# Kernel tuning notes

Measured on AMD Instinct MI355X. Metric: run time of the kernel, lower is better.

Reference implementation:

```python
import jax, jax.numpy as jnp
import numpy as np
from math import factorial

N_NODES = 20000
N_EDGES = 80000
NUM_GRAPHS = 64
NUM_NEIGHBORS = 3.8
POOL_NODES = 4.0  # num_nodes=4 constant in source forward

# ---------------- real Wigner 3j (e3nn-style, Frobenius norm 1) ----------------

def _w3j_complex(j1, j2, j3, m1, m2, m3):
    if m1 + m2 + m3 != 0:
        return 0.0
    t1 = j2 - m1 - j3; t2 = j1 + m2 - j3; t3 = j1 + j2 - j3
    t4 = j1 - m1; t5 = j2 + m2
    tmin = max(0, t1, t2); tmax = min(t3, t4, t5)
    if tmin > tmax:
        return 0.0
    s = 0.0
    for t in range(tmin, tmax + 1):
        s += (-1.0) ** t / (factorial(t) * factorial(t - t1) * factorial(t - t2)
                            * factorial(t3 - t) * factorial(t4 - t) * factorial(t5 - t))
    tri = (factorial(j1 + j2 - j3) * factorial(j1 - j2 + j3) * factorial(-j1 + j2 + j3)
           / factorial(j1 + j2 + j3 + 1))
    norm = np.sqrt(tri * factorial(j1 + m1) * factorial(j1 - m1) * factorial(j2 + m2)
                   * factorial(j2 - m2) * factorial(j3 + m3) * factorial(j3 - m3))
    return (-1.0) ** (j1 - j2 - m3) * norm * s


def _real_basis(l):
    U = np.zeros((2 * l + 1, 2 * l + 1), dtype=np.complex128)
    U[l, l] = 1.0
    for m in range(1, l + 1):
        U[l + m, l + m] = (-1) ** m / np.sqrt(2.0)
        U[l + m, l - m] = 1.0 / np.sqrt(2.0)
        U[l - m, l - m] = 1j / np.sqrt(2.0)
        U[l - m, l + m] = -1j * (-1) ** m / np.sqrt(2.0)
    return U

_W3J_CACHE = {}

def w3j(l1, l2, l3):
    key = (l1, l2, l3)
    if key not in _W3J_CACHE:
        C = np.zeros((2 * l1 + 1, 2 * l2 + 1, 2 * l3 + 1), dtype=np.complex128)
        for m1 in range(-l1, l1 + 1):
            for m2 in range(-l2, l2 + 1):
                m3 = -(m1 + m2)
                if -l3 <= m3 <= l3:
                    C[m1 + l1, m2 + l2, m3 + l3] = _w3j_complex(l1, l2, l3, m1, m2, m3)
        C = np.einsum('ia,jb,kc,abc->ijk', _real_basis(l1), _real_basis(l2), _real_basis(l3), C)
        C = np.real((-1j) ** (l1 + l2 + l3) * C)
        _W3J_CACHE[key] = jnp.asarray(C, dtype=jnp.float32)
    return _W3J_CACHE[key]

# ---------------- irreps bookkeeping ----------------
SH        = [(1, 0, 1), (1, 1, -1), (1, 2, 1), (1, 3, -1)]            # 1x0e+1x1o+1x2e+1x3o (dim 16)
GATE1_IN  = [(16,0,1),(16,0,-1),(8,0,1),(8,0,-1),(8,0,1),(8,0,-1),(16,1,-1),(16,1,1)]  # dim 160
GATE1_OUT = [(16,0,1),(16,0,1),(16,1,-1),(16,1,1)]                     # dim 128
GATE2_IN  = [(16,0,1),(16,0,-1),(6,0,1),(6,0,-1),(6,0,1),(6,0,-1),(12,1,-1),(12,1,1)]  # dim 128
GATE2_OUT = [(16,0,1),(16,0,1),(12,1,-1),(12,1,1)]                     # dim 104
OUT_FINAL = [(1, 0, 1)]


def slices(irreps):
    out = []; o = 0
    for m, l, p in irreps:
        d = m * (2 * l + 1); out.append((o, o + d)); o += d
    return out


def tp_paths(ir1, ir2, iro):
    paths = []
    for i1, (m1, l1, p1) in enumerate(ir1):
        for i2, (m2, l2, p2) in enumerate(ir2):
            for io, (mo, lo, po) in enumerate(iro):
                if po == p1 * p2 and abs(l1 - l2) <= lo <= l1 + l2:
                    paths.append((i1, i2, io))
    fan = [0] * len(iro)
    for i1, i2, io in paths:
        fan[io] += ir1[i1][0] * ir2[i2][0]
    numel = sum(ir1[i1][0] * ir2[i2][0] * iro[io][0] for i1, i2, io in paths)
    return paths, fan, numel


def tensor_product(x1, x2, weights, ir1, ir2, iro):
    # FullyConnectedTensorProduct, component norm, element path normalization
    paths, fan, numel = tp_paths(ir1, ir2, iro)
    s1, s2 = slices(ir1), slices(ir2)
    E = x1.shape[0]
    out_parts = [jnp.zeros((E, m * (2 * l + 1)), x1.dtype) for m, l, p in iro]
    wofs = 0
    for i1, i2, io in paths:
        m1, l1, _ = ir1[i1]; m2, l2, _ = ir2[i2]; mo, lo, _ = iro[io]
        n = m1 * m2 * mo
        w = weights[:, wofs:wofs + n].reshape(E, m1, m2, mo); wofs += n
        a = x1[:, s1[i1][0]:s1[i1][1]].reshape(E, m1, 2 * l1 + 1)
        b = x2[:, s2[i2][0]:s2[i2][1]].reshape(E, m2, 2 * l2 + 1)
        C = w3j(l1, l2, lo)
        pw = np.sqrt((2 * lo + 1) / fan[io])
        seg = jnp.einsum('eui,evj,ijk,euvw->ewk', a, b, C, w) * pw
        out_parts[io] = out_parts[io] + seg.reshape(E, mo * (2 * lo + 1))
    return jnp.concatenate(out_parts, axis=1)

# ---------------- activations / gate ----------------
_xs = np.linspace(-8.0, 8.0, 100001)
_pdf = np.exp(-0.5 * _xs ** 2) / np.sqrt(2 * np.pi)
TANH_NORM = float(1.0 / np.sqrt(np.sum(np.tanh(_xs) ** 2 * _pdf) * (_xs[1] - _xs[0])))
SQRT2 = float(np.sqrt(2.0))
ACT = {'relu': lambda t: jnp.maximum(t, 0.0) * SQRT2,
       'abs':  lambda t: jnp.abs(t),
       'tanh': lambda t: jnp.tanh(t) * TANH_NORM}


def gate_fn(x, scalars, gates, gated):
    o = 0; outs = []
    for m, a in scalars:
        outs.append(ACT[a](x[:, o:o + m])); o += m
    gv = []
    for m, a in gates:
        gv.append(ACT[a](x[:, o:o + m])); o += m
    g = jnp.concatenate(gv, axis=-1)
    gi = 0
    for m, l in gated:
        d = 2 * l + 1
        feat = x[:, o:o + m * d].reshape(-1, m, d)
        outs.append((feat * g[:, gi:gi + m, None]).reshape(-1, m * d))
        o += m * d; gi += m
    return jnp.concatenate(outs, axis=-1)

# ---------------- edge features ----------------

def sh_component(v):
    # real spherical harmonics l=0..3, 'component' normalization, unit input
    x, y, z = v[:, 0], v[:, 1], v[:, 2]
    s3, s5, s15 = np.sqrt(3.0), np.sqrt(5.0), np.sqrt(15.0)
    s7, s42, s70, s105 = np.sqrt(7.0), np.sqrt(42.0), np.sqrt(70.0), np.sqrt(105.0)
    Y0 = jnp.ones_like(x)[:, None]
    Y1 = jnp.stack([s3 * y, s3 * z, s3 * x], -1)
    Y2 = jnp.stack([s15 * x * y, s15 * y * z, 0.5 * s5 * (3 * z * z - 1.0),
                    s15 * x * z, 0.5 * s15 * (x * x - y * y)], -1)
    Y3 = jnp.stack([0.25 * s70 * y * (3 * x * x - y * y), s105 * x * y * z,
                    0.25 * s42 * y * (5 * z * z - 1.0), 0.5 * s7 * z * (5 * z * z - 3.0),
                    0.25 * s42 * x * (5 * z * z - 1.0), 0.5 * s105 * z * (x * x - y * y),
                    0.25 * s70 * x * (x * x - 3 * y * y)], -1)
    return jnp.concatenate([Y0, Y1, Y2, Y3], -1)  # [E,16]


def soft_one_hot(r):
    # soft_one_hot_linspace(start=0.5,end=2.5,number=3,basis='smooth_finite',cutoff=True)
    values = np.linspace(0.5, 2.5, 5)[1:-1]
    step = values[1] - values[0]
    diff = (r[:, None] - values) / step
    def f(u):
        return jnp.where(u > 0, jnp.exp(-1.0 / jnp.where(u > 0, u, 1.0)), 0.0)
    y = 1.14136 * np.exp(2.0) * f(diff + 1.0) * f(1.0 - diff)
    return y * np.sqrt(3.0)


def fc(x, w1, w2):
    # e3nn FullyConnectedNet([3,256,numel], relu)
    h = jnp.maximum(x @ (w1 / np.sqrt(w1.shape[0])), 0.0) * SQRT2
    return h @ (w2 / np.sqrt(w2.shape[0]))


def convolution(node_feats, edge_src, edge_dst, edge_attr, edge_scalars, w1, w2, ir_in, ir_out, n_nodes):
    weight = fc(edge_scalars, w1, w2)                                   # [E, numel]
    ef = tensor_product(node_feats[edge_src], edge_attr, weight, ir_in, SH, ir_out)
    return jax.ops.segment_sum(ef, edge_dst, num_segments=n_nodes) / np.sqrt(NUM_NEIGHBORS)


def _forward(pos, w1_1, w2_1, w1_2, w2_2, w1_3, w2_3, edge_src, edge_dst, batch):
    N = pos.shape[0]
    vec = pos[edge_src] - pos[edge_dst]
    r = jnp.sqrt(jnp.sum(vec * vec, axis=1) + 1e-12)
    unit = vec / r[:, None]
    edge_attr = sh_component(unit)
    edge_scalars = soft_one_hot(r)
    x = jax.ops.segment_sum(edge_attr, edge_dst, num_segments=N) / np.sqrt(NUM_NEIGHBORS)
    x = convolution(x, edge_src, edge_dst, edge_attr, edge_scalars, w1_1, w2_1, SH, GATE1_IN, N)
    x = gate_fn(x, [(16, 'relu'), (16, 'abs')], [(8, 'relu'), (8, 'tanh'), (8, 'relu'), (8, 'tanh')], [(16, 1), (16, 1)])
    x = convolution(x, edge_src, edge_dst, edge_attr, edge_scalars, w1_2, w2_2, GATE1_OUT, GATE2_IN, N)
    x = gate_fn(x, [(16, 'relu'), (16, 'abs')], [(6, 'relu'), (6, 'tanh'), (6, 'relu'), (6, 'tanh')], [(12, 1), (12, 1)])
    x = convolution(x, edge_src, edge_dst, edge_attr, edge_scalars, w1_3, w2_3, GATE2_OUT, OUT_FINAL, N)
    x = jax.ops.segment_sum(x, batch, num_segments=NUM_GRAPHS) / np.sqrt(POOL_NODES)
    return jax.nn.sigmoid(x)


def setup_inputs():
    key = jax.random.key(0)
    ks = jax.random.split(key, 10)
    pos = jax.random.normal(ks[0], (N_NODES, 3), jnp.float32) * 1.5
    edge_src = jax.random.randint(ks[1], (N_EDGES,), 0, N_NODES)
    edge_dst = jax.random.randint(ks[2], (N_EDGES,), 0, N_NODES)
    batch = jnp.sort(jax.random.randint(ks[3], (N_NODES,), 0, NUM_GRAPHS))
    _, _, n1 = tp_paths(SH, SH, GATE1_IN)
    _, _, n2 = tp_paths(GATE1_OUT, SH, GATE2_IN)
    _, _, n3 = tp_paths(GATE2_OUT, SH, OUT_FINAL)
    w1_1 = jax.random.normal(ks[4], (3, 256), jnp.float32)
    w2_1 = jax.random.normal(ks[5], (256, n1), jnp.float32)
    w1_2 = jax.random.normal(ks[6], (3, 256), jnp.float32)
    w2_2 = jax.random.normal(ks[7], (256, n2), jnp.float32)
    w1_3 = jax.random.normal(ks[8], (3, 256), jnp.float32)
    w2_3 = jax.random.normal(ks[9], (256, n3), jnp.float32)
    return {'pos': pos, 'w1_1': w1_1, 'w2_1': w2_1, 'w1_2': w1_2, 'w2_2': w2_2,
            'w1_3': w1_3, 'w2_3': w2_3, 'edge_src': edge_src, 'edge_dst': edge_dst, 'batch': batch}


def reference(pos, w1_1, w2_1, w1_2, w2_2, w1_3, w2_3, edge_src, edge_dst, batch):
    return _forward(pos, w1_1, w2_1, w1_2, w2_2, w1_3, w2_3, edge_src, edge_dst, batch)
```

## Files before the change

### kernel.cpp

```cpp
#include <hip/hip_runtime.h>
#include <math.h>

#define NNODE 20000
#define NEDGE 80000
#define NGRAPH 64

#define OFF_TANH  656
#define OFF_CNT   660
#define OFF_GSUM  664
#define OFF_HIST  7680
#define OFF_OFFS  9728
#define OFF_CUR   11784
#define OFF_EATTR 14336
#define OFF_RBUF  1294336
#define OFF_EINFO 1374336
#define OFF_X0    1694336
#define OFF_Y1    2014336
#define OFF_Y2    5214336
#define OFF_X1    7774336
#define OFF_X2    10334336
#define OFF_TAB   12414336

#define T000 0
#define T110 1
// ... 277 lines not shown
__constant__ ColMetaT< 1,  3,  44> CMETA3 = gen_colmeta_< 1,  3,  44>(OSEG3, HPATHS3, HCORES3);

struct CItem { short aoff, boff, n1, n2, cofs, jstep, woff, pad; };
struct CArr1 { CItem it[31]; };
constexpr CArr1 gen_c1_(){
  CArr1 a{}; int s=0;
  for(int cn=0;cn<13;cn++){
    CoreD cd=HCORES1[cn];
    int n1=2*cd.l1+1,n2=2*cd.l2+1,n3=2*cd.l3+1;
    for(int k=0;k<n3;k++){
      a.it[s]=CItem{cd.a_off,cd.b_off,(short)n1,(short)n2,(short)(cd.tab+k),(short)n3,(short)(cd.coff+k),0};
      s++;
    }
  }
  return a;
}
__constant__ CArr1 CIT1 = gen_c1_();

struct Fam { short b_off, tab, n1, n2, n3, goff; };
constexpr Fam GF2[6]={
  {0,T000,1,1,1,0},{1,T011,1,3,3,1},{0,T101,3,1,3,4},
  {1,T110,3,3,1,13},{1,T111,3,3,3,16},{4,T121,3,5,3,25}};
constexpr Fam GF3[2]={{0,T000,1,1,1,0},{1,T110,3,3,1,1}};
struct CoreG { short fam,a_off,m1,coff; };
constexpr CoreG CG2[12]={
  {0,0,16,0},{1,0,16,16},{0,16,16,64},{1,16,16,80},
  {2,32,16,128},{3,32,16,176},{4,32,16,192},{5,32,16,240},
  {2,80,16,288},{3,80,16,336},{4,80,16,352},{5,80,16,400}};
constexpr CoreG CG3[3]={{0,0,16,0},{0,16,16,16},{1,32,12,32}};

struct GItem { short boff, cofs, n2, jstep; };
template<int NG> struct GArrT { GItem it[NG]; };
template<int NG,int NF>
constexpr GArrT<NG> gen_g_(const Fam (&F)[NF]){
  GArrT<NG> a{}; int s=0;
  for(int f=0;f<NF;f++){
    for(int i=0;i<F[f].n1;i++)for(int k=0;k<F[f].n3;k++){
      a.it[s]=GItem{F[f].b_off,(short)(F[f].tab + i*F[f].n2*F[f].n3 + k),F[f].n2,F[f].n3};
      s++;
    }
  }
  return a;
}
__constant__ GArrT<34> GIT2=gen_g_<34>(GF2);
__constant__ GArrT<4>  GIT3=gen_g_<4>(GF3);

struct OItem { short aoff, gofs, n1, n3, woff, pad; };
template<int NO> struct OArrT { OItem it[NO]; };
template<int NO,int NC,int NF>
constexpr OArrT<NO> gen_o_(const CoreG (&C)[NC], const Fam (&F)[NF]){
  OArrT<NO> a{}; int s=0;
  for(int cn=0;cn<NC;cn++){
    Fam f=F[C[cn].fam];
    for(int k=0;k<f.n3;k++)for(int u=0;u<C[cn].m1;u++){
      a.it[s]=OItem{(short)(C[cn].a_off+u*f.n1),(short)(f.goff+k),f.n1,f.n3,
                    (short)(C[cn].coff+k*C[cn].m1+u),0};
      s++;
    }
  }
  return a;
}
__constant__ OArrT<448> OIT2=gen_o_<448,12,6>(CG2,GF2);
__constant__ OArrT<44>  OIT3=gen_o_<44,3,2>(CG3,GF3);

template<int CNT,int N3,int NCOLS>
__device__ __forceinline__ void apply1_col(const Ent2* __restrict__ ep, const float* __restrict__ T0,
    const float* __restrict__ crb, float fr, float&a0,float&a1,float&a2){
  const float* tja=T0+ep[0].jb;
  float wv[CNT];
  #pragma unroll
  for(int t=0;t<CNT;t++){
    float w0=tja[t], w1=tja[t+NCOLS];
    wv[t]=w0+fr*(w1-w0);
  }
  #pragma unroll
  for(int t=0;t<CNT;t++){
    const float* cr=crb+ep[t].cb;
    a0=fmaf(wv[t],cr[0],a0);
    if constexpr(N3==3){ a1=fmaf(wv[t],cr[1],a1); a2=fmaf(wv[t],cr[2],a2); }
  }
}
__device__ __forceinline__ void apply1_dyn(const Ent2* __restrict__ ep, int cnt, int n3,
    const float* __restrict__ T0, const float* __restrict__ crb, float fr, int NCOLS,
    float&a0,float&a1,float&a2){
  const float* tja=T0+ep[0].jb;
  for(int t=0;t<cnt;t++){
    float w0=tja[t], w1=tja[t+NCOLS];
    float w=w0+fr*(w1-w0);
    const float* cr=crb+ep[t].cb;
    a0=fmaf(w,cr[0],a0);
    if(n3==3){ a1=fmaf(w,cr[1],a1); a2=fmaf(w,cr[2],a2); }
  }
}
template<int CNT,int N3,int NCOLS>
__device__ __forceinline__ void apply2_col(const Ent2* __restrict__ ep, const float* __restrict__ T0,
    const float* __restrict__ crb, float fr, float&a0,float&a1,float&a2){
  #pragma unroll
  for(int t=0;t<CNT;t++){
    const float* cr=crb+ep[t].cb;
    const float* tj=T0+ep[t].jb;
    #pragma unroll
    for(int uu=0;uu<16;uu+=4){
      float4 w0=*(const float4*)(tj+uu);
      float4 w1=*(const float4*)(tj+NCOLS+uu);
      float w;
      if constexpr(N3==1){
        float4 cv=*(const float4*)(cr+uu);
        w=w0.x+fr*(w1.x-w0.x); a0=fmaf(w,cv.x,a0);
        w=w0.y+fr*(w1.y-w0.y); a0=fmaf(w,cv.y,a0);
        w=w0.z+fr*(w1.z-w0.z); a0=fmaf(w,cv.z,a0);
        w=w0.w+fr*(w1.w-w0.w); a0=fmaf(w,cv.w,a0);
      } else {
        float4 c0=*(const float4*)(cr+uu);
        float4 c1=*(const float4*)(cr+16+uu);
        float4 c2=*(const float4*)(cr+32+uu);
        w=w0.x+fr*(w1.x-w0.x); a0=fmaf(w,c0.x,a0); a1=fmaf(w,c1.x,a1); a2=fmaf(w,c2.x,a2);
        w=w0.y+fr*(w1.y-w0.y); a0=fmaf(w,c0.y,a0); a1=fmaf(w,c1.y,a1); a2=fmaf(w,c2.y,a2);
        w=w0.z+fr*(w1.z-w0.z); a0=fmaf(w,c0.z,a0); a1=fmaf(w,c1.z,a1); a2=fmaf(w,c2.z,a2);
        w=w0.w+fr*(w1.w-w0.w); a0=fmaf(w,c0.w,a0); a1=fmaf(w,c1.w,a1); a2=fmaf(w,c2.w,a2);
      }
    }
  }
}
__device__ __forceinline__ void apply2_dyn(const Ent2* __restrict__ ep, int cnt, int n3,
    const float* __restrict__ T0, const float* __restrict__ crb, float fr, int NCOLS,
    float&a0,float&a1,float&a2){
  for(int t=0;t<cnt;t++){
    const float* cr=crb+ep[t].cb;
    const float* tj=T0+ep[t].jb;
    #pragma unroll
    for(int uu=0;uu<16;uu+=4){
      float4 w0=*(const float4*)(tj+uu);
      float4 w1=*(const float4*)(tj+NCOLS+uu);
      float w;
      if(n3==1){
        float4 cv=*(const float4*)(cr+uu);
        w=w0.x+fr*(w1.x-w0.x); a0=fmaf(w,cv.x,a0);
        w=w0.y+fr*(w1.y-w0.y); a0=fmaf(w,cv.y,a0);
        w=w0.z+fr*(w1.z-w0.z); a0=fmaf(w,cv.z,a0);
        w=w0.w+fr*(w1.w-w0.w); a0=fmaf(w,cv.w,a0);
      } else {
        float4 c0=*(const float4*)(cr+uu);
        float4 c1=*(const float4*)(cr+16+uu);
        float4 c2=*(const float4*)(cr+32+uu);
        w=w0.x+fr*(w1.x-w0.x); a0=fmaf(w,c0.x,a0); a1=fmaf(w,c1.x,a1); a2=fmaf(w,c2.x,a2);
        w=w0.y+fr*(w1.y-w0.y); a0=fmaf(w,c0.y,a0); a1=fmaf(w,c1.y,a1); a2=fmaf(w,c2.y,a2);
        w=w0.z+fr*(w1.z-w0.z); a0=fmaf(w,c0.z,a0); a1=fmaf(w,c1.z,a1); a2=fmaf(w,c2.z,a2);
        w=w0.w+fr*(w1.w-w0.w); a0=fmaf(w,c0.w,a0); a1=fmaf(w,c1.w,a1); a2=fmaf(w,c2.w,a2);
      }
    }
  }
}

template<int JT>
__device__ __forceinline__ void ldw_(float* w, const float* p){
  if constexpr(JT==2) *(float2*)w = *(const float2*)p;
  else if constexpr(JT==4) *(float4*)w = *(const float4*)p;
  else { *(float4*)w=*(const float4*)p; *(float4*)(w+4)=*(const float4*)(p+4); }
}
template<int JT>
__device__ __forceinline__ void table_gemm(const float* __restrict__ W2, float* __restrict__ tab,
    int NCOLS, float scale, const float* __restrict__ PW, const int* __restrict__ NJ,
    int jb, const float (*__restrict__ sh_h)[8], int r0, int R){
  float acc[8][JT];
  #pragma unroll
  for(int k=0;k<8;k++)
    #pragma unroll
    for(int u=0;u<JT;u++) acc[k][u]=0.0f;
  const float* w2p=W2+jb;
  float w0[JT], w1[JT];
  ldw_<JT>(w0, w2p);
  ldw_<JT>(w1, w2p+NCOLS);
  for(int c=0;c<256;c+=2){
    int cp0=(c+2<256)?(c+2):255;
    int cp1=(c+3<256)?(c+3):255;
    float n0[JT], n1[JT];
    ldw_<JT>(n0, w2p+(size_t)cp0*NCOLS);
    ldw_<JT>(n1, w2p+(size_t)cp1*NCOLS);
    float h0[8], h1[8];
    *(float4*)&h0[0]=*(const float4*)&sh_h[c][0];
    *(float4*)&h0[4]=*(const float4*)&sh_h[c][4];
    *(float4*)&h1[0]=*(const float4*)&sh_h[c+1][0];
    *(float4*)&h1[4]=*(const float4*)&sh_h[c+1][4];
    #pragma unroll
    for(int k=0;k<8;k++)
      #pragma unroll
      for(int u=0;u<JT;u++)
        acc[k][u]=fmaf(h0[k],w0[u],acc[k][u]);
    #pragma unroll
    for(int k=0;k<8;k++)
      #pragma unroll
      for(int u=0;u<JT;u++)
        acc[k][u]=fmaf(h1[k],w1[u],acc[k][u]);
    #pragma unroll
    for(int u=0;u<JT;u++){ w0[u]=n0[u]; w1[u]=n1[u]; }
  }
  #pragma unroll
  for(int u=0;u<JT;u++){
    float cs=scale*PW[jb+u];
    int jn=NJ[jb+u];
    #pragma unroll
    for(int k=0;k<8;k++){
      int ri=r0+k;
      if(ri<R) tab[(size_t)ri*NCOLS+jn]=acc[k][u]*cs;
    }
  }
}

__global__ __launch_bounds__(256) void k_front(
    const float* __restrict__ W1_1, const float* __restrict__ W2_1, float* __restrict__ T1,
    const float* __restrict__ W1_2, const float* __restrict__ W2_2, float* __restrict__ T2,
    const float* __restrict__ W1_3, const float* __restrict__ W2_3, float* __restrict__ T3,
    const float* __restrict__ pos, const int* __restrict__ esrc, const int* __restrict__ edst,
    int R, int NR, int NXT, float* __restrict__ ws){
  __shared__ float sh_h[256][8];
  int bid=blockIdx.x;
  int tid=threadIdx.x;
  int NT2=7*NXT;

  if(bid<NT2+2*NXT){
    int jb0, jlim, xt;
    const float* W1; const float* W2; float* tab; int NCOLS; float scale;
    const float* PW; const int* NJ;
    if(bid<NT2){
      int s=bid/NXT; xt=bid-s*NXT; jb0=s*512; jlim=(jb0+512<3328)?(jb0+512):3328;
      W1=W1_2; W2=W2_2; tab=T2; NCOLS=3328; scale=INV_SQRT_NEIGH; PW=PWC2.v; NJ=CMETA2.newj;
    } else if(bid<NT2+NXT){
      xt=bid-NT2; jb0=0; jlim=272;
      W1=W1_1; W2=W2_1; tab=T1; NCOLS=272; scale=INV_SQRT_NEIGH; PW=PWC1.v; NJ=CMETA1.newj;
    } else {
      xt=bid-NT2-NXT; jb0=0; jlim=44;
      W1=W1_3; W2=W2_3; tab=T3; NCOLS=44; scale=INV_SQRT_NEIGH*0.5f; PW=PWC3.v; NJ=CMETA3.newj;
    }
    int r0=xt*8;
    {
      int c=tid;
      float wa=W1[c], wb=W1[256+c], wc=W1[512+c];
      const float A=(float)(1.14136*7.38905609893065*1.7320508075688772);
      #pragma unroll
      for(int k=0;k<8;k++){
        int ri=r0+k;
        float r=0.5f+2.0f*(float)ri/(float)NR;
        float sv[3];
        #pragma unroll
        for(int j=0;j<3;j++){
          float v=1.0f+0.5f*(float)j;
          float diff=(r-v)*2.0f;
          float u1=diff+1.0f, u2=1.0f-diff;
          float f1=(u1>0.0f)? expf(-1.0f/u1):0.0f;
          float f2=(u2>0.0f)? expf(-1.0f/u2):0.0f;
          sv[j]=A*f1*f2;
        }
        float hv=sv[0]*wa+sv[1]*wb+sv[2]*wc;
        hv=fmaxf(hv*0.5773502691896258f,0.0f)*(SQRT2F*0.0625f);
        sh_h[c][k]=hv;
      }
    }
    __syncthreads();
    int jb=jb0+tid*2;
    if(jb+2<=jlim)
      table_gemm<2>(W2,tab,NCOLS,scale,PW,NJ,jb,sh_h,r0,R);
    return;
  }
  bid-=NT2+2*NXT;

  if(bid==0){
    __shared__ double red[256];
    double loc=0.0;
    for(int i=tid;i<=100000;i+=256){
      float x=-8.0f+16.0f*(float)i/100000.0f;
      float th=tanhf(x);
      float pdf=expf(-0.5f*x*x)*0.3989422804014327f;
      loc += (double)(th*th*pdf);
    }
    red[tid]=loc; __syncthreads();
    for(int s=128;s>0;s>>=1){ if(tid<s) red[tid]+=red[tid+s]; __syncthreads(); }
    if(tid==0) ws[OFF_TANH]=(float)(1.0/sqrt(red[0]*(16.0/100000.0)));
    return;
  }
  bid-=1;

  if(bid<313){
    int e=bid*256+tid;
    if(e>=NEDGE) return;
    float* eattr=ws+OFF_EATTR;
    float* x0=ws+OFF_X0;
    int s=esrc[e], d=edst[e];
    float x=pos[3*s]-pos[3*d], y=pos[3*s+1]-pos[3*d+1], z=pos[3*s+2]-pos[3*d+2];
    float r=sqrtf(x*x+y*y+z*z+1e-12f);
    float iv=1.0f/r; x*=iv; y*=iv; z*=iv;
    const float s3=1.7320508075688772f, s5=2.2360679774997896f, s15=3.872983346207417f;
    const float s7=2.6457513110645907f, s42=6.48074069840786f, s70=8.366600265340756f, s105=10.246950765959598f;
    float Y[16];
    Y[0]=1.0f;
    Y[1]=s3*y; Y[2]=s3*z; Y[3]=s3*x;
    Y[4]=s15*x*y; Y[5]=s15*y*z; Y[6]=0.5f*s5*(3.0f*z*z-1.0f); Y[7]=s15*x*z; Y[8]=0.5f*s15*(x*x-y*y);
    Y[9]=0.25f*s70*y*(3.0f*x*x-y*y); Y[10]=s105*x*y*z; Y[11]=0.25f*s42*y*(5.0f*z*z-1.0f);
    Y[12]=0.5f*s7*z*(5.0f*z*z-3.0f); Y[13]=0.25f*s42*x*(5.0f*z*z-1.0f);
    Y[14]=0.5f*s105*z*(x*x-y*y); Y[15]=0.25f*s70*x*(x*x-3.0f*y*y);
    float4* ep=(float4*)(eattr+(size_t)e*16);
    ep[0]=make_float4(Y[0],Y[1],Y[2],Y[3]);
    ep[1]=make_float4(Y[4],Y[5],Y[6],Y[7]);
    ep[2]=make_float4(Y[8],Y[9],Y[10],Y[11]);
    ep[3]=make_float4(Y[12],Y[13],Y[14],Y[15]);
    #pragma unroll
    for(int i=0;i<16;i++)
      atomicAdd(&x0[(size_t)d*16+i], Y[i]*INV_SQRT_NEIGH);
    ws[OFF_RBUF+e]=r;
    if(r>0.5f && r<2.5f){
      float t=(r-0.5f)*((float)NR*0.5f);
      int i0=min((int)t, NR-1);
      atomicAdd((int*)(ws+OFF_HIST)+i0, 1);
    }
    return;
  }
  bid-=313;

  {
    float4* dst=(float4*)(ws+OFF_Y1);
    size_t n4=(size_t)(OFF_X1-OFF_Y1)/4;
    float4 z4=make_float4(0.f,0.f,0.f,0.f);
    for(size_t i=(size_t)bid*256+tid; i<n4; i+=(size_t)256*256)
      dst[i]=z4;
  }
}

__global__ void k_scan(float* __restrict__ ws, int NR){
  __shared__ int sd[2048];
  int t=threadIdx.x;
  int* hist=(int*)(ws+OFF_HIST);
  int* offs=(int*)(ws+OFF_OFFS);
  int i1=t, i2=t+1024;
  sd[i1]=(i1<NR)? hist[i1]:0;
  sd[i2]=(i2<NR)? hist[i2]:0;
  __syncthreads();
  for(int d=1; d<2048; d<<=1){
    int v1=(i1>=d)? sd[i1-d]:0;
    int v2=(i2>=d)? sd[i2-d]:0;
    __syncthreads();
    sd[i1]+=v1; sd[i2]+=v2;
    __syncthreads();
  }
  if(i1<NR) offs[i1]=(i1==0)?0:sd[i1-1];
  if(i2<NR) offs[i2]=sd[i2-1];
  if(t==0){ offs[NR]=sd[NR-1]; *((int*)(ws+OFF_CNT))=sd[NR-1]; }
}

__global__ void k_scatter(const int* __restrict__ esrc, const int* __restrict__ edst,
                          float* __restrict__ ws, int NR){
  int e=blockIdx.x*256+threadIdx.x;
  if(e>=NEDGE) return;
  float r=ws[OFF_RBUF+e];
  if(!(r>0.5f && r<2.5f)) return;
  float t=(r-0.5f)*((float)NR*0.5f);
  int i0=min((int)t, NR-1);
  int* offs=(int*)(ws+OFF_OFFS);
  int* cur=(int*)(ws+OFF_CUR);
  int p=offs[i0]+atomicAdd(&cur[i0],1);
  int4 v; v.x=esrc[e]; v.y=edst[e]; v.z=e; v.w=__float_as_int(t);
  ((int4*)(ws+OFF_EINFO))[p]=v;
}

template<int CONV,int DY,int D_IN,int D_OUT,int CSTRIDE,int NCOL,int NCOLS,bool FINAL>
__global__ __launch_bounds__(256,4) void k_conv(
    const float* __restrict__ xin, const float* __restrict__ TAB,
    float* __restrict__ yout, const int* __restrict__ batchp,
    float* __restrict__ ws, int NR)
{
  constexpr int APAD = D_IN+4;
  constexpr int NGP  = (CONV==2)?36:4;
  constexpr int YST  = (CONV==3)?132:4;
  constexpr int NGV  = (CONV==2)?32:((CONV==3)?24:1);
  __shared__ float sh_a[8][APAD];
  __shared__ float sh_b[8][20];
  __shared__ float sh_core[8][CSTRIDE];
  __shared__ float sh_g[8][NGP];
  __shared__ float sh_gv[8][NGV];
  __shared__ float sh_y[8][YST];
  __shared__ float sh_red[8];
  __shared__ int sh_src[8], sh_dst[8], sh_eid[8];
  __shared__ float sh_t[8];

  int tid=threadIdx.x;
  int nact=*(const int*)(ws+OFF_CNT);
  int base=blockIdx.x*8;
  if(base>=nact) return;
  int ne=min(8, nact-base);

  if(tid<8){
    int src=0,dst=0,eid=-1; float tv=0.0f;
    if(tid<ne){
      int4 v=((const int4*)(ws+OFF_EINFO))[base+tid];
      src=v.x; dst=v.y; eid=v.z; tv=__int_as_float(v.w);
    }
    sh_src[tid]=src; sh_dst[tid]=dst; sh_eid[tid]=eid; sh_t[tid]=tv;
    if constexpr(CONV==3) sh_red[tid]=0.0f;
  }
  __syncthreads();

  if(tid<32){
    int idx=tid>>2, c4=tid&3;
    int eid=sh_eid[idx];
    float4 v=make_float4(0.f,0.f,0.f,0.f);
    if(eid>=0) v=((const float4*)(ws+OFF_EATTR+(size_t)eid*16))[c4];
    *(float4*)&sh_b[idx][c4*4]=v;
  }
  if constexpr(CONV==1){
    if(tid>=32 && tid<64){
      int t2=tid-32; int idx=t2>>2, c4=t2&3;
      float4 v=make_float4(0.f,0.f,0.f,0.f);
      if(sh_eid[idx]>=0) v=((const float4*)(xin+(size_t)sh_src[idx]*16))[c4];
      *(float4*)&sh_a[idx][c4*4]=v;
    }
  } else {
    constexpr int YQ=DY/4;
    for(int z=tid; z<8*YQ; z+=256){
      int idx=z/YQ, c4=z-idx*YQ;
      float4 v=make_float4(0.f,0.f,0.f,0.f);
      if(sh_eid[idx]>=0) v=((const float4*)(xin+(size_t)sh_src[idx]*DY))[c4];
      if constexpr(CONV==2) *(float4*)&sh_core[idx][c4*4]=v;
      else                  *(float4*)&sh_y[idx][c4*4]=v;
    }
  }
  __syncthreads();

  if constexpr(CONV==1){
    constexpr int NIT=31;
    for(int z=tid; z<8*NIT; z+=256){
      int idx=z/NIT, rem=z-idx*NIT;
      CItem it=CIT1.it[rem];
      float acc=0.0f;
      for(int i=0;i<it.n1;i++){
        float av=sh_a[idx][it.aoff+i];
        int cb=it.cofs + i*it.n2*it.jstep;
        for(int j=0;j<it.n2;j++)
          acc += av*sh_b[idx][it.boff+j]*W3JC.v[cb + j*it.jstep];
      }
      sh_core[idx][it.woff]=acc;
    }
    __syncthreads();
  } else {
    float TN=ws[OFF_TANH];
    for(int z=tid; z<8*NGV; z+=256){
      int idx=z/NGV, m=z-idx*NGV;
      const float* yr=(CONV==2)? &sh_core[idx][0] : &sh_y[idx][0];
      float u=yr[32+m];
      bool th=(CONV==2)? (((m>>3)&1)!=0) : (((m/6)&1)!=0);
      sh_gv[idx][m]= th? tanhf(u)*TN : fmaxf(u,0.0f)*SQRT2F;
    }
    constexpr int NG=(CONV==2)?34:4;
    for(int z=tid; z<8*NG; z+=256){
      int idx=z/NG, rem=z-idx*NG;
      GItem it=(CONV==2)? GIT2.it[rem] : GIT3.it[rem];
      float acc=0.0f;
      for(int j=0;j<it.n2;j++)
        acc += sh_b[idx][it.boff+j]*W3JC.v[it.cofs + j*it.jstep];
      sh_g[idx][rem]=acc;
    }
    __syncthreads();
    for(int z=tid; z<8*D_IN; z+=256){
      int idx=z/D_IN, o=z-idx*D_IN;
      const float* yr=(CONV==2)? &sh_core[idx][0] : &sh_y[idx][0];
      float val;
      if(o<16) val=fmaxf(yr[o],0.0f)*SQRT2F;
      else if(o<32) val=fabsf(yr[o]);
      else {
        if constexpr(CONV==2){
          int gi=(o<80)? (o-32)/3 : 16+(o-80)/3;
          val=yr[o+32]*sh_gv[idx][gi];
        } else {
          int gi=(o<68)? (o-32)/3 : 12+(o-68)/3;
          val=yr[o+24]*sh_gv[idx][gi];
        }
      }
      sh_a[idx][o]=val;
    }
    __syncthreads();
    constexpr int NO=(CONV==2)?448:44;
    for(int z=tid; z<8*NO; z+=256){
      int idx=z/NO, rem=z-idx*NO;
      OItem it=(CONV==2)? OIT2.it[rem] : OIT3.it[rem];
      float acc=0.0f;
      #pragma unroll 3
      for(int i=0;i<it.n1;i++)
        acc += sh_a[idx][it.aoff+i]*sh_g[idx][it.gofs + i*it.n3];
      sh_core[idx][it.woff]=acc;
    }
    __syncthreads();
  }

  if constexpr(CONV==3){
    if(tid<88){
      int e3=tid&7, c=tid>>3;
      float tv=sh_t[e3];
      int i0=min((int)tv, NR-1);
      float fr=tv-(float)i0;
      const float* tj=TAB+(size_t)i0*NCOLS + c*4;
      float4 w0=*(const float4*)tj;
      float4 w1=*(const float4*)(tj+NCOLS);
      float4 cv=*(const float4*)(&sh_core[e3][c*4]);
      float p;
      p  = (w0.x+fr*(w1.x-w0.x))*cv.x;
      p += (w0.y+fr*(w1.y-w0.y))*cv.y;
      p += (w0.z+fr*(w1.z-w0.z))*cv.z;
      p += (w0.w+fr*(w1.w-w0.w))*cv.w;
      atomicAdd(&sh_red[e3], p);
    }
    __syncthreads();
    if(tid<ne) atomicAdd(&ws[OFF_GSUM+batchp[sh_dst[tid]]], sh_red[tid]);
  } else {
    int e=tid&7;
    float tv=sh_t[e];
    int i0=min((int)tv, NR-1);
    float fr=tv-(float)i0;
    const float* T0=TAB+(size_t)i0*NCOLS;
    const float* crb=&sh_core[e][0];
    int dstv=sh_dst[e];
    bool act=(e<ne);

    for(int q=tid; q<8*NCOL; q+=256){
      int c=q>>3;
      int s0,s1,ob,n3;
      const Ent2* entp;
      if constexpr(CONV==1){ s0=CMETA1.cidx[c]; s1=CMETA1.cidx[c+1]; ob=CMETA1.obase[c]; n3=CMETA1.n3c[c]; entp=CMETA1.ent; }
      else                 { s0=CMETA2.cidx[c]; s1=CMETA2.cidx[c+1]; ob=CMETA2.obase[c]; n3=CMETA2.n3c[c]; entp=CMETA2.ent; }
      int cnt=s1-s0;
      if(!cnt) continue;
      float a0=0.0f,a1=0.0f,a2=0.0f;
      const Ent2* ep=entp+s0;
      if constexpr(CONV==1){
        if(n3==1){
          switch(cnt){
            case 4: apply1_col<4,1,272>(ep,T0,crb,fr,a0,a1,a2); break;
            default: apply1_dyn(ep,cnt,1,T0,crb,fr,272,a0,a1,a2); break;
          }
        } else {
          switch(cnt){
            case 6: apply1_col<6,3,272>(ep,T0,crb,fr,a0,a1,a2); break;
            case 3: apply1_col<3,3,272>(ep,T0,crb,fr,a0,a1,a2); break;
            default: apply1_dyn(ep,cnt,3,T0,crb,fr,272,a0,a1,a2); break;
          }
        }
      } else {
        if(n3==1){
          switch(cnt){
            case 3: apply2_col<3,1,3328>(ep,T0,crb,fr,a0,a1,a2); break;
            case 1: apply2_col<1,1,3328>(ep,T0,crb,fr,a0,a1,a2); break;
            default: apply2_dyn(ep,cnt,1,T0,crb,fr,3328,a0,a1,a2); break;
          }
        } else {
          switch(cnt){
            case 5: apply2_col<5,3,3328>(ep,T0,crb,fr,a0,a1,a2); break;
            case 3: apply2_col<3,3,3328>(ep,T0,crb,fr,a0,a1,a2); break;
            default: apply2_dyn(ep,cnt,3,T0,crb,fr,3328,a0,a1,a2); break;
          }
        }
      }
      if(act){
        float* yp=&yout[(size_t)dstv*D_OUT+ob];
        atomicAdd(yp, a0);
        if(n3==3){ atomicAdd(yp+1, a1); atomicAdd(yp+2, a2); }
      }
    }
  }
}

__global__ void k_sig(const float* __restrict__ ws, float* __restrict__ out){
  int g=threadIdx.x;
  if(g<NGRAPH){
    float v=ws[OFF_GSUM+g];
    out[g]=1.0f/(1.0f+expf(-v));
  }
}

extern "C" void kernel_launch(void* const* d_in, const int* in_sizes, int n_in,
                              void* d_out, int out_size, void* d_ws, size_t ws_size,
                              hipStream_t stream){
  const float* pos =(const float*)d_in[0];
  const float* w1_1=(const float*)d_in[1];
  const float* w2_1=(const float*)d_in[2];
  const float* w1_2=(const float*)d_in[3];
  const float* w2_2=(const float*)d_in[4];
  const float* w1_3=(const float*)d_in[5];
  const float* w2_3=(const float*)d_in[6];
  const int* esrc=(const int*)d_in[7];
  const int* edst=(const int*)d_in[8];
  const int* batch=(const int*)d_in[9];
  float* ws=(float*)d_ws;
  float* out=(float*)d_out;

  long availRows = ((long)(ws_size/4) - (long)OFF_TAB)/3644L;
  int R = (availRows < 1025L)? (int)availRows : 1025;
  if(R < 9) R = 9;
  int NR = R-1;
  int NXT = (R+7)/8;
  float* TAB1 = ws + OFF_TAB;
  float* TAB2 = TAB1 + (size_t)R*272;
  float* TAB3 = TAB2 + (size_t)R*3328;

  hipMemsetAsync(ws+OFF_CNT, 0, (size_t)(728-OFF_CNT)*sizeof(float), stream);
  hipMemsetAsync(ws+OFF_HIST, 0, (size_t)(13832-OFF_HIST)*sizeof(float), stream);
  hipMemsetAsync(ws+OFF_X0, 0, (size_t)(OFF_Y1-OFF_X0)*sizeof(float), stream);

  int nblk = 9*NXT + 1 + 313 + 256;
  k_front<<<nblk,256,0,stream>>>(
      w1_1,w2_1,TAB1, w1_2,w2_2,TAB2, w1_3,w2_3,TAB3,
      pos, esrc, edst, R, NR, NXT, ws);
  k_scan<<<1,1024,0,stream>>>(ws, NR);
  k_scatter<<<(NEDGE+255)/256,256,0,stream>>>(esrc, edst, ws, NR);

  k_conv<1, 16, 16,160, 33, 96, 272,false><<<(NEDGE+7)/8,256,0,stream>>>(
      ws+OFF_X0, TAB1, ws+OFF_Y1, batch, ws, NR);

  k_conv<2,160,128,128,452, 80,3328,false><<<(NEDGE+7)/8,256,0,stream>>>(
      ws+OFF_Y1, TAB2, ws+OFF_Y2, batch, ws, NR);

  k_conv<3,128,104,  1, 68,  1, 44,true ><<<(NEDGE+7)/8,256,0,stream>>>(
      ws+OFF_Y2, TAB3, nullptr, batch, ws, NR);

  k_sig<<<1,64,0,stream>>>(ws, out);
}
```

Before: 338.1 us.

## Move layer-2/3 table builds into conv1 kernel to overlap with edge work

```diff
diff --git a/kernel.cpp b/kernel.cpp
--- a/kernel.cpp
+++ b/kernel.cpp
@@ -508,62 +508,52 @@
   }
 }
 
-__global__ __launch_bounds__(256) void k_front(
+__device__ __forceinline__ void table_role(const float* __restrict__ W1, const float* __restrict__ W2,
+    float* __restrict__ tab, int NCOLS, float scale, const float* __restrict__ PW,
+    const int* __restrict__ NJ, int jb0, int jlim, int r0, int R, int NR,
+    float (*__restrict__ sh_h)[8], int tid){
+  {
+    int c=tid;
+    float wa=W1[c], wb=W1[256+c], wc=W1[512+c];
+    const float A=(float)(1.14136*7.38905609893065*1.7320508075688772);
+    #pragma unroll
+    for(int k=0;k<8;k++){
+      int ri=r0+k;
+      float r=0.5f+2.0f*(float)ri/(float)NR;
+      float sv[3];
+      #pragma unroll
+      for(int j=0;j<3;j++){
+        float v=1.0f+0.5f*(float)j;
+        float diff=(r-v)*2.0f;
+        float u1=diff+1.0f, u2=1.0f-diff;
+        float f1=(u1>0.0f)? expf(-1.0f/u1):0.0f;
+        float f2=(u2>0.0f)? expf(-1.0f/u2):0.0f;
+        sv[j]=A*f1*f2;
+      }
+      float hv=sv[0]*wa+sv[1]*wb+sv[2]*wc;
+      hv=fmaxf(hv*0.5773502691896258f,0.0f)*(SQRT2F*0.0625f);
+      sh_h[c][k]=hv;
+    }
+  }
+  __syncthreads();
+  int jb=jb0+tid*2;
+  if(jb+2<=jlim)
+    table_gemm<2>(W2,tab,NCOLS,scale,PW,NJ,jb,sh_h,r0,R);
+}
+
+__global__ __launch_bounds__(256) void k_front_a(
     const float* __restrict__ W1_1, const float* __restrict__ W2_1, float* __restrict__ T1,
-    const float* __restrict__ W1_2, const float* __restrict__ W2_2, float* __restrict__ T2,
-    const float* __restrict__ W1_3, const float* __restrict__ W2_3, float* __restrict__ T3,
     const float* __restrict__ pos, const int* __restrict__ esrc, const int* __restrict__ edst,
     int R, int NR, int NXT, float* __restrict__ ws){
   __shared__ float sh_h[256][8];
   int bid=blockIdx.x;
   int tid=threadIdx.x;
-  int NT2=7*NXT;
-
-  if(bid<NT2+2*NXT){
-    int jb0, jlim, xt;
-    const float* W1; const float* W2; float* tab; int NCOLS; float scale;
-    const float* PW; const int* NJ;
-    if(bid<NT2){
-      int s=bid/NXT; xt=bid-s*NXT; jb0=s*512; jlim=(jb0+512<3328)?(jb0+512):3328;
-      W1=W1_2; W2=W2_2; tab=T2; NCOLS=3328; scale=INV_SQRT_NEIGH; PW=PWC2.v; NJ=CMETA2.newj;
-    } else if(bid<NT2+NXT){
-      xt=bid-NT2; jb0=0; jlim=272;
-      W1=W1_1; W2=W2_1; tab=T1; NCOLS=272; scale=INV_SQRT_NEIGH; PW=PWC1.v; NJ=CMETA1.newj;
-    } else {
-      xt=bid-NT2-NXT; jb0=0; jlim=44;
-      W1=W1_3; W2=W2_3; tab=T3; NCOLS=44; scale=INV_SQRT_NEIGH*0.5f; PW=PWC3.v; NJ=CMETA3.newj;
-    }
-    int r0=xt*8;
-    {
-      int c=tid;
-      float wa=W1[c], wb=W1[256+c], wc=W1[512+c];
-      const float A=(float)(1.14136*7.38905609893065*1.7320508075688772);
-      #pragma unroll
-      for(int k=0;k<8;k++){
-        int ri=r0+k;
-        float r=0.5f+2.0f*(float)ri/(float)NR;
-        float sv[3];
-        #pragma unroll
-        for(int j=0;j<3;j++){
-          float v=1.0f+0.5f*(float)j;
-          float diff=(r-v)*2.0f;
-          float u1=diff+1.0f, u2=1.0f-diff;
-          float f1=(u1>0.0f)? expf(-1.0f/u1):0.0f;
-          float f2=(u2>0.0f)? expf(-1.0f/u2):0.0f;
-          sv[j]=A*f1*f2;
-        }
-        float hv=sv[0]*wa+sv[1]*wb+sv[2]*wc;
-        hv=fmaxf(hv*0.5773502691896258f,0.0f)*(SQRT2F*0.0625f);
-        sh_h[c][k]=hv;
-      }
-    }
-    __syncthreads();
-    int jb=jb0+tid*2;
-    if(jb+2<=jlim)
-      table_gemm<2>(W2,tab,NCOLS,scale,PW,NJ,jb,sh_h,r0,R);
+
+  if(bid<NXT){
+    table_role(W1_1,W2_1,T1,272,INV_SQRT_NEIGH,PWC1.v,CMETA1.newj,0,272,bid*8,R,NR,sh_h,tid);
     return;
   }
-  bid-=NT2+2*NXT;
+  bid-=NXT;
 
   if(bid==0){
     __shared__ double red[256];
@@ -662,6 +652,122 @@
   ((int4*)(ws+OFF_EINFO))[p]=v;
 }
 
+__global__ __launch_bounds__(256,4) void k_conv1t(
+    const float* __restrict__ W1_2, const float* __restrict__ W2_2, float* __restrict__ T2,
+    const float* __restrict__ W1_3, const float* __restrict__ W2_3, float* __restrict__ T3,
+    const float* __restrict__ xin, const float* __restrict__ TAB,
+    float* __restrict__ yout, float* __restrict__ ws, int R, int NR, int NXT)
+{
+  __shared__ float sh_h[256][8];
+  int bid=blockIdx.x;
+  int tid=threadIdx.x;
+  int NT2=7*NXT;
+
+  if(bid<NT2+NXT){
+    if(bid<NT2){
+      int s=bid/NXT; int xt=bid-s*NXT; int jb0=s*512;
+      int jlim=(jb0+512<3328)?(jb0+512):3328;
+      table_role(W1_2,W2_2,T2,3328,INV_SQRT_NEIGH,PWC2.v,CMETA2.newj,jb0,jlim,xt*8,R,NR,sh_h,tid);
+    } else {
+      int xt=bid-NT2;
+      table_role(W1_3,W2_3,T3,44,INV_SQRT_NEIGH*0.5f,PWC3.v,CMETA3.newj,0,44,xt*8,R,NR,sh_h,tid);
+    }
+    return;
+  }
+  bid-=NT2+NXT;
+
+  __shared__ float sh_a[8][20];
+  __shared__ float sh_b[8][20];
+  __shared__ float sh_core[8][33];
+  __shared__ int sh_src[8], sh_dst[8], sh_eid[8];
+  __shared__ float sh_t[8];
+
+  int nact=*(const int*)(ws+OFF_CNT);
+  int base=bid*8;
+  if(base>=nact) return;
+  int ne=min(8, nact-base);
+
+  if(tid<8){
+    int src=0,dst=0,eid=-1; float tv=0.0f;
+    if(tid<ne){
+      int4 v=((const int4*)(ws+OFF_EINFO))[base+tid];
+      src=v.x; dst=v.y; eid=v.z; tv=__int_as_float(v.w);
+    }
+    sh_src[tid]=src; sh_dst[tid]=dst; sh_eid[tid]=eid; sh_t[tid]=tv;
+  }
+  __syncthreads();
+
+  if(tid<32){
+    int idx=tid>>2, c4=tid&3;
+    int eid=sh_eid[idx];
+    float4 v=make_float4(0.f,0.f,0.f,0.f);
+    if(eid>=0) v=((const float4*)(ws+OFF_EATTR+(size_t)eid*16))[c4];
+    *(float4*)&sh_b[idx][c4*4]=v;
+  }
+  if(tid>=32 && tid<64){
+    int t2=tid-32; int idx=t2>>2, c4=t2&3;
+    float4 v=make_float4(0.f,0.f,0.f,0.f);
+    if(sh_eid[idx]>=0) v=((const float4*)(xin+(size_t)sh_src[idx]*16))[c4];
+    *(float4*)&sh_a[idx][c4*4]=v;
+  }
+  __syncthreads();
+
+  {
+    constexpr int NIT=31;
+    for(int z=tid; z<8*NIT; z+=256){
+      int idx=z/NIT, rem=z-idx*NIT;
+      CItem it=CIT1.it[rem];
+      float acc=0.0f;
+      for(int i=0;i<it.n1;i++){
+        float av=sh_a[idx][it.aoff+i];
+        int cb=it.cofs + i*it.n2*it.jstep;
+        for(int j=0;j<it.n2;j++)
+          acc += av*sh_b[idx][it.boff+j]*W3JC.v[cb + j*it.jstep];
+      }
+      sh_core[idx][it.woff]=acc;
+    }
+    __syncthreads();
+  }
+
+  {
+    int e=tid&7;
+    float tv=sh_t[e];
+    int i0=min((int)tv, NR-1);
+    float fr=tv-(float)i0;
+    const float* T0=TAB+(size_t)i0*272;
+    const float* crb=&sh_core[e][0];
+    int dstv=sh_dst[e];
+    bool act=(e<ne);
+
+    for(int q=tid; q<8*96; q+=256){
+      int c=q>>3;
+      int s0=CMETA1.cidx[c], s1=CMETA1.cidx[c+1];
+      int ob=CMETA1.obase[c], n3=CMETA1.n3c[c];
+      int cnt=s1-s0;
+      if(!cnt) continue;
+      float a0=0.0f,a1=0.0f,a2=0.0f;
+      const Ent2* ep=CMETA1.ent+s0;
+      if(n3==1){
+        switch(cnt){
+          case 4: apply1_col<4,1,272>(ep,T0,crb,fr,a0,a1,a2); break;
+          default: apply1_dyn(ep,cnt,1,T0,crb,fr,272,a0,a1,a2); break;
+        }
+      } else {
+        switch(cnt){
+          case 6: apply1_col<6,3,272>(ep,T0,crb,fr,a0,a1,a2); break;
+          case 3: apply1_col<3,3,272>(ep,T0,crb,fr,a0,a1,a2); break;
+          default: apply1_dyn(ep,cnt,3,T0,crb,fr,272,a0,a1,a2); break;
+        }
+      }
+      if(act){
+        float* yp=&yout[(size_t)dstv*160+ob];
+        atomicAdd(yp, a0);
+        if(n3==3){ atomicAdd(yp+1, a1); atomicAdd(yp+2, a2); }
+      }
+    }
+  }
+}
+
 template<int CONV,int DY,int D_IN,int D_OUT,int CSTRIDE,int NCOL,int NCOLS,bool FINAL>
 __global__ __launch_bounds__(256,4) void k_conv(
     const float* __restrict__ xin, const float* __restrict__ TAB,
@@ -706,14 +812,7 @@
     if(eid>=0) v=((const float4*)(ws+OFF_EATTR+(size_t)eid*16))[c4];
     *(float4*)&sh_b[idx][c4*4]=v;
   }
-  if constexpr(CONV==1){
-    if(tid>=32 && tid<64){
-      int t2=tid-32; int idx=t2>>2, c4=t2&3;
-      float4 v=make_float4(0.f,0.f,0.f,0.f);
-      if(sh_eid[idx]>=0) v=((const float4*)(xin+(size_t)sh_src[idx]*16))[c4];
-      *(float4*)&sh_a[idx][c4*4]=v;
-    }
-  } else {
+  {
     constexpr int YQ=DY/4;
     for(int z=tid; z<8*YQ; z+=256){
       int idx=z/YQ, c4=z-idx*YQ;
@@ -725,22 +824,7 @@
   }
   __syncthreads();
 
-  if constexpr(CONV==1){
-    constexpr int NIT=31;
-    for(int z=tid; z<8*NIT; z+=256){
-      int idx=z/NIT, rem=z-idx*NIT;
-      CItem it=CIT1.it[rem];
-      float acc=0.0f;
-      for(int i=0;i<it.n1;i++){
-        float av=sh_a[idx][it.aoff+i];
-        int cb=it.cofs + i*it.n2*it.jstep;
-        for(int j=0;j<it.n2;j++)
-          acc += av*sh_b[idx][it.boff+j]*W3JC.v[cb + j*it.jstep];
-      }
-      sh_core[idx][it.woff]=acc;
-    }
-    __syncthreads();
-  } else {
+  {
     float TN=ws[OFF_TANH];
     for(int z=tid; z<8*NGV; z+=256){
       int idx=z/NGV, m=z-idx*NGV;
@@ -821,40 +905,23 @@
 
     for(int q=tid; q<8*NCOL; q+=256){
       int c=q>>3;
-      int s0,s1,ob,n3;
-      const Ent2* entp;
-      if constexpr(CONV==1){ s0=CMETA1.cidx[c]; s1=CMETA1.cidx[c+1]; ob=CMETA1.obase[c]; n3=CMETA1.n3c[c]; entp=CMETA1.ent; }
-      else                 { s0=CMETA2.cidx[c]; s1=CMETA2.cidx[c+1]; ob=CMETA2.obase[c]; n3=CMETA2.n3c[c]; entp=CMETA2.ent; }
+      int s0=CMETA2.cidx[c], s1=CMETA2.cidx[c+1];
+      int ob=CMETA2.obase[c], n3=CMETA2.n3c[c];
       int cnt=s1-s0;
       if(!cnt) continue;
       float a0=0.0f,a1=0.0f,a2=0.0f;
-      const Ent2* ep=entp+s0;
-      if constexpr(CONV==1){
-        if(n3==1){
-          switch(cnt){
-            case 4: apply1_col<4,1,272>(ep,T0,crb,fr,a0,a1,a2); break;
-            default: apply1_dyn(ep,cnt,1,T0,crb,fr,272,a0,a1,a2); break;
-          }
-        } else {
-          switch(cnt){
-            case 6: apply1_col<6,3,272>(ep,T0,crb,fr,a0,a1,a2); break;
-            case 3: apply1_col<3,3,272>(ep,T0,crb,fr,a0,a1,a2); break;
-            default: apply1_dyn(ep,cnt,3,T0,crb,fr,272,a0,a1,a2); break;
-          }
+      const Ent2* ep=CMETA2.ent+s0;
+      if(n3==1){
+        switch(cnt){
+          case 3: apply2_col<3,1,3328>(ep,T0,crb,fr,a0,a1,a2); break;
+          case 1: apply2_col<1,1,3328>(ep,T0,crb,fr,a0,a1,a2); break;
+          default: apply2_dyn(ep,cnt,1,T0,crb,fr,3328,a0,a1,a2); break;
         }
       } else {
-        if(n3==1){
-          switch(cnt){
-            case 3: apply2_col<3,1,3328>(ep,T0,crb,fr,a0,a1,a2); break;
-            case 1: apply2_col<1,1,3328>(ep,T0,crb,fr,a0,a1,a2); break;
-            default: apply2_dyn(ep,cnt,1,T0,crb,fr,3328,a0,a1,a2); break;
-          }
-        } else {
-          switch(cnt){
-            case 5: apply2_col<5,3,3328>(ep,T0,crb,fr,a0,a1,a2); break;
-            case 3: apply2_col<3,3,3328>(ep,T0,crb,fr,a0,a1,a2); break;
-            default: apply2_dyn(ep,cnt,3,T0,crb,fr,3328,a0,a1,a2); break;
-          }
+        switch(cnt){
+          case 5: apply2_col<5,3,3328>(ep,T0,crb,fr,a0,a1,a2); break;
+          case 3: apply2_col<3,3,3328>(ep,T0,crb,fr,a0,a1,a2); break;
+          default: apply2_dyn(ep,cnt,3,T0,crb,fr,3328,a0,a1,a2); break;
         }
       }
       if(act){
@@ -903,15 +970,14 @@
   hipMemsetAsync(ws+OFF_HIST, 0, (size_t)(13832-OFF_HIST)*sizeof(float), stream);
   hipMemsetAsync(ws+OFF_X0, 0, (size_t)(OFF_Y1-OFF_X0)*sizeof(float), stream);
 
-  int nblk = 9*NXT + 1 + 313 + 256;
-  k_front<<<nblk,256,0,stream>>>(
-      w1_1,w2_1,TAB1, w1_2,w2_2,TAB2, w1_3,w2_3,TAB3,
-      pos, esrc, edst, R, NR, NXT, ws);
+  k_front_a<<<NXT+1+313+256,256,0,stream>>>(
+      w1_1,w2_1,TAB1, pos, esrc, edst, R, NR, NXT, ws);
   k_scan<<<1,1024,0,stream>>>(ws, NR);
   k_scatter<<<(NEDGE+255)/256,256,0,stream>>>(esrc, edst, ws, NR);
 
-  k_conv<1, 16, 16,160, 33, 96, 272,false><<<(NEDGE+7)/8,256,0,stream>>>(
-      ws+OFF_X0, TAB1, ws+OFF_Y1, batch, ws, NR);
+  k_conv1t<<<8*NXT+(NEDGE+7)/8,256,0,stream>>>(
+      w1_2,w2_2,TAB2, w1_3,w2_3,TAB3,
+      ws+OFF_X0, TAB1, ws+OFF_Y1, ws, R, NR, NXT);
 
   k_conv<2,160,128,128,452, 80,3328,false><<<(NEDGE+7)/8,256,0,stream>>>(
       ws+OFF_Y1, TAB2, ws+OFF_Y2, batch, ws, NR);
```

After: 343.5 us. No clear change (+1.6%).

## Split table GEMM reduction across two thread halves and narrow column groups

Applied to the files above, without the earlier changes.

```diff
diff --git a/kernel.cpp b/kernel.cpp
--- a/kernel.cpp
+++ b/kernel.cpp
@@ -453,58 +453,38 @@
   }
 }
 
-template<int JT>
-__device__ __forceinline__ void ldw_(float* w, const float* p){
-  if constexpr(JT==2) *(float2*)w = *(const float2*)p;
-  else if constexpr(JT==4) *(float4*)w = *(const float4*)p;
-  else { *(float4*)w=*(const float4*)p; *(float4*)(w+4)=*(const float4*)(p+4); }
-}
-template<int JT>
-__device__ __forceinline__ void table_gemm(const float* __restrict__ W2, float* __restrict__ tab,
-    int NCOLS, float scale, const float* __restrict__ PW, const int* __restrict__ NJ,
-    int jb, const float (*__restrict__ sh_h)[8], int r0, int R){
-  float acc[8][JT];
+__device__ __forceinline__ void table_accum_half(const float* __restrict__ W2,
+    int NCOLS, int jb, const float (*__restrict__ sh_h)[8], int c0,
+    float (&acc)[8][2]){
   #pragma unroll
-  for(int k=0;k<8;k++)
-    #pragma unroll
-    for(int u=0;u<JT;u++) acc[k][u]=0.0f;
+  for(int k=0;k<8;k++){ acc[k][0]=0.0f; acc[k][1]=0.0f; }
   const float* w2p=W2+jb;
-  float w0[JT], w1[JT];
-  ldw_<JT>(w0, w2p);
-  ldw_<JT>(w1, w2p+NCOLS);
-  for(int c=0;c<256;c+=2){
+  float w0[2], w1[2];
+  *(float2*)w0 = *(const float2*)(w2p+(size_t)c0*NCOLS);
+  *(float2*)w1 = *(const float2*)(w2p+(size_t)(c0+1)*NCOLS);
+  int cend=c0+128;
+  for(int c=c0; c<cend; c+=2){
     int cp0=(c+2<256)?(c+2):255;
     int cp1=(c+3<256)?(c+3):255;
-    float n0[JT], n1[JT];
-    ldw_<JT>(n0, w2p+(size_t)cp0*NCOLS);
-    ldw_<JT>(n1, w2p+(size_t)cp1*NCOLS);
+    float n0[2], n1[2];
+    *(float2*)n0 = *(const float2*)(w2p+(size_t)cp0*NCOLS);
+    *(float2*)n1 = *(const float2*)(w2p+(size_t)cp1*NCOLS);
     float h0[8], h1[8];
     *(float4*)&h0[0]=*(const float4*)&sh_h[c][0];
     *(float4*)&h0[4]=*(const float4*)&sh_h[c][4];
     *(float4*)&h1[0]=*(const float4*)&sh_h[c+1][0];
     *(float4*)&h1[4]=*(const float4*)&sh_h[c+1][4];
     #pragma unroll
-    for(int k=0;k<8;k++)
-      #pragma unroll
-      for(int u=0;u<JT;u++)
-        acc[k][u]=fmaf(h0[k],w0[u],acc[k][u]);
-    #pragma unroll
-    for(int k=0;k<8;k++)
-      #pragma unroll
-      for(int u=0;u<JT;u++)
-        acc[k][u]=fmaf(h1[k],w1[u],acc[k][u]);
-    #pragma unroll
-    for(int u=0;u<JT;u++){ w0[u]=n0[u]; w1[u]=n1[u]; }
-  }
-  #pragma unroll
-  for(int u=0;u<JT;u++){
-    float cs=scale*PW[jb+u];
-    int jn=NJ[jb+u];
+    for(int k=0;k<8;k++){
+      acc[k][0]=fmaf(h0[k],w0[0],acc[k][0]);
+      acc[k][1]=fmaf(h0[k],w0[1],acc[k][1]);
+    }
     #pragma unroll
     for(int k=0;k<8;k++){
-      int ri=r0+k;
-      if(ri<R) tab[(size_t)ri*NCOLS+jn]=acc[k][u]*cs;
-    }
+      acc[k][0]=fmaf(h1[k],w1[0],acc[k][0]);
+      acc[k][1]=fmaf(h1[k],w1[1],acc[k][1]);
+    }
+    w0[0]=n0[0]; w0[1]=n0[1]; w1[0]=n1[0]; w1[1]=n1[1];
   }
 }
 
@@ -515,24 +495,21 @@
     const float* __restrict__ pos, const int* __restrict__ esrc, const int* __restrict__ edst,
     int R, int NR, int NXT, float* __restrict__ ws){
   __shared__ float sh_h[256][8];
+  __shared__ float sh_x[128][16];
   int bid=blockIdx.x;
   int tid=threadIdx.x;
-  int NT2=7*NXT;
-
-  if(bid<NT2+2*NXT){
-    int jb0, jlim, xt;
+  int NTB=16*NXT;
+
+  if(bid<NTB){
+    int g=bid/NXT, xt=bid-g*NXT;
     const float* W1; const float* W2; float* tab; int NCOLS; float scale;
-    const float* PW; const int* NJ;
-    if(bid<NT2){
-      int s=bid/NXT; xt=bid-s*NXT; jb0=s*512; jlim=(jb0+512<3328)?(jb0+512):3328;
-      W1=W1_2; W2=W2_2; tab=T2; NCOLS=3328; scale=INV_SQRT_NEIGH; PW=PWC2.v; NJ=CMETA2.newj;
-    } else if(bid<NT2+NXT){
-      xt=bid-NT2; jb0=0; jlim=272;
-      W1=W1_1; W2=W2_1; tab=T1; NCOLS=272; scale=INV_SQRT_NEIGH; PW=PWC1.v; NJ=CMETA1.newj;
-    } else {
-      xt=bid-NT2-NXT; jb0=0; jlim=44;
-      W1=W1_3; W2=W2_3; tab=T3; NCOLS=44; scale=INV_SQRT_NEIGH*0.5f; PW=PWC3.v; NJ=CMETA3.newj;
-    }
+    const float* PW; const int* NJ; int jb0, jlim;
+    if(g<13){ W1=W1_2; W2=W2_2; tab=T2; NCOLS=3328; scale=INV_SQRT_NEIGH;
+              PW=PWC2.v; NJ=CMETA2.newj; jb0=g*256; jlim=jb0+256; }
+    else if(g<15){ W1=W1_1; W2=W2_1; tab=T1; NCOLS=272; scale=INV_SQRT_NEIGH;
+              PW=PWC1.v; NJ=CMETA1.newj; jb0=(g-13)*256; jlim=272; }
+    else { W1=W1_3; W2=W2_3; tab=T3; NCOLS=44; scale=INV_SQRT_NEIGH*0.5f;
+              PW=PWC3.v; NJ=CMETA3.newj; jb0=0; jlim=44; }
     int r0=xt*8;
     {
       int c=tid;
@@ -558,12 +535,32 @@
       }
     }
     __syncthreads();
-    int jb=jb0+tid*2;
-    if(jb+2<=jlim)
-      table_gemm<2>(W2,tab,NCOLS,scale,PW,NJ,jb,sh_h,r0,R);
+    int cp=tid&127, h=tid>>7;
+    int jb=jb0+cp*2;
+    bool active=(jb+2<=jlim);
+    int jbs=active? jb : jb0;
+    float acc[8][2];
+    table_accum_half(W2, NCOLS, jbs, sh_h, h*128, acc);
+    if(h==1){
+      #pragma unroll
+      for(int k=0;k<8;k++){ sh_x[cp][k*2]=acc[k][0]; sh_x[cp][k*2+1]=acc[k][1]; }
+    }
+    __syncthreads();
+    if(h==0 && active){
+      #pragma unroll
+      for(int u=0;u<2;u++){
+        float cs=scale*PW[jb+u];
+        int jn=NJ[jb+u];
+        #pragma unroll
+        for(int k=0;k<8;k++){
+          int ri=r0+k;
+          if(ri<R) tab[(size_t)ri*NCOLS+jn]=(acc[k][u]+sh_x[cp][k*2+u])*cs;
+        }
+      }
+    }
     return;
   }
-  bid-=NT2+2*NXT;
+  bid-=NTB;
 
   if(bid==0){
     __shared__ double red[256];
@@ -903,7 +900,7 @@
   hipMemsetAsync(ws+OFF_HIST, 0, (size_t)(13832-OFF_HIST)*sizeof(float), stream);
   hipMemsetAsync(ws+OFF_X0, 0, (size_t)(OFF_Y1-OFF_X0)*sizeof(float), stream);
 
-  int nblk = 9*NXT + 1 + 313 + 256;
+  int nblk = 16*NXT + 1 + 313 + 256;
   k_front<<<nblk,256,0,stream>>>(
       w1_1,w2_1,TAB1, w1_2,w2_2,TAB2, w1_3,w2_3,TAB3,
       pos, esrc, edst, R, NR, NXT, ws);
```

After: 341.8 us. About the same (+1.1%).
